# Performance work log

Hardware: AMD Instinct MI355X
Metric: run time of the kernel (lower is better)

The kernel has to match this reference:

```python
import jax, jax.numpy as jnp
import numpy as np

N_AST, M, C, D, H, OUT = 200000, 400000, 25000, 256, 4, 256


def setup_inputs() -> dict:
    key = jax.random.key(0)
    ks = jax.random.split(key, 12)
    s = 0.02
    return {
        "ast_nodes_encodings": jax.random.normal(ks[0], (N_AST, D), jnp.float32),
        "ast_node_idx_to_pdg_node_idx_mapping_key": jax.random.randint(ks[1], (M,), 0, N_AST),
        "ast_node_idx_to_pdg_node_idx_mapping_value": jax.random.randint(ks[2], (M,), 0, C),
        "pdg_node_idx_to_sub_ast_root_idx_mapping_key": jax.random.randint(ks[3], (C,), 0, C),
        "pdg_node_idx_to_sub_ast_root_idx_mapping_value": jax.random.randint(ks[4], (C,), 0, N_AST),
        "nr_cfg_nodes": C,
        "Wq": jax.random.normal(ks[5], (D, D), jnp.float32) * s,
        "bq": jnp.zeros((D,), jnp.float32),
        "Wk": jax.random.normal(ks[6], (D, D), jnp.float32) * s,
        "bk": jnp.zeros((D,), jnp.float32),
        "Wv": jax.random.normal(ks[7], (D, D), jnp.float32) * s,
        "bv": jnp.zeros((D,), jnp.float32),
        "Wo": jax.random.normal(ks[8], (D, OUT), jnp.float32) * s,
        "bo": jnp.zeros((OUT,), jnp.float32),
    }


def _scatter_attn(x, attn_keys, seg, num_segments, Wq, bq, Wk, bk, Wv, bv, Wo, bo):
    # x: [M, D] scattered inputs; attn_keys: [C, D] per-segment queries; seg: [M] segment ids.
    d_h = D // H
    q = (attn_keys @ Wq + bq).reshape(num_segments, H, d_h)  # [C,H,dh]
    k = (x @ Wk + bk).reshape(-1, H, d_h)                    # [M,H,dh]
    v = (x @ Wv + bv).reshape(-1, H, d_h)                    # [M,H,dh]
    scale = 1.0 / jnp.sqrt(jnp.asarray(d_h, x.dtype))
    scores = jnp.einsum('mhd,mhd->mh', k, q[seg]) * scale    # [M,H]
    m = jax.ops.segment_max(scores, seg, num_segments=num_segments)  # [C,H]
    e = jnp.exp(scores - m[seg])                             # [M,H]
    denom = jax.ops.segment_sum(e, seg, num_segments=num_segments)  # [C,H]
    num = jax.ops.segment_sum((e[..., None] * v).reshape(-1, H * d_h),
                              seg, num_segments=num_segments)        # [C,D]
    pooled = (num.reshape(num_segments, H, d_h) / (denom[..., None] + 1e-9)).reshape(num_segments, D)
    return pooled @ Wo + bo                                  # [C,OUT]


def reference(ast_nodes_encodings,
              ast_node_idx_to_pdg_node_idx_mapping_key,
              ast_node_idx_to_pdg_node_idx_mapping_value,
              pdg_node_idx_to_sub_ast_root_idx_mapping_key,
              pdg_node_idx_to_sub_ast_root_idx_mapping_value,
              nr_cfg_nodes, Wq, bq, Wk, bk, Wv, bv, Wo, bo):
    # Build per-CFG-node attention keys: gather sub-AST-root encodings, scatter by PDG node idx.
    root_enc = ast_nodes_encodings[pdg_node_idx_to_sub_ast_root_idx_mapping_value]  # [C,D]
    attn_keys = jnp.zeros((nr_cfg_nodes, D), ast_nodes_encodings.dtype)
    attn_keys = attn_keys.at[pdg_node_idx_to_sub_ast_root_idx_mapping_key].set(root_enc)
    # Gather AST node encodings per mapping entry and attention-pool per CFG node.
    scattered = ast_nodes_encodings[ast_node_idx_to_pdg_node_idx_mapping_key]       # [M,D]
    return _scatter_attn(scattered, attn_keys, ast_node_idx_to_pdg_node_idx_mapping_value,
                         nr_cfg_nodes, Wq, bq, Wk, bk, Wv, bv, Wo, bo)
```

## Files before the change

### kernel.cpp

```cpp
#include <hip/hip_runtime.h>
#include <hip/hip_bf16.h>
#include <math.h>

#define D 256
#define H 4
#define DH 64
#define NOUT 256

typedef short bf16x8 __attribute__((ext_vector_type(8)));
typedef float f32x4 __attribute__((ext_vector_type(4)));

__device__ __forceinline__ ushort f2bf(float f){
  uint b = __float_as_uint(f);
  b += 0x7FFF + ((b >> 16) & 1);
  return (ushort)(b >> 16);
}

__device__ __forceinline__ float redux32(float v){
  int t;
  t = __builtin_amdgcn_update_dpp(0, __float_as_int(v), 0x121, 0xF, 0xF, true); v += __int_as_float(t);
  t = __builtin_amdgcn_update_dpp(0, __float_as_int(v), 0x122, 0xF, 0xF, true); v += __int_as_float(t);
  t = __builtin_amdgcn_update_dpp(0, __float_as_int(v), 0x124, 0xF, 0xF, true); v += __int_as_float(t);
  t = __builtin_amdgcn_update_dpp(0, __float_as_int(v), 0x128, 0xF, 0xF, true); v += __int_as_float(t);
  v += __shfl_xor(v, 16, 64);
  return v;
}

__global__ void count_winner_kernel(const int* __restrict__ seg, int* __restrict__ counts,
                                    const int* __restrict__ pdgkey, int* __restrict__ winner,
                                    int M, int C){
  int i = blockIdx.x*256 + threadIdx.x;
  if (i < M){ int s = seg[i]; if (s >= 0 && s < C) atomicAdd(&counts[s], 1); }
  if (i < C){ int t = pdgkey[i]; if (t >= 0 && t < C) atomicMax(&winner[t], i); }
}

__global__ __launch_bounds__(1024) void scan1_kernel(const int* __restrict__ counts,
    int* __restrict__ loc, int* __restrict__ btot, int C){
  __shared__ int wtot[16];
  __shared__ int wexcl[16];
  int tid = threadIdx.x, lane = tid & 63, wv = tid >> 6;
  int i = blockIdx.x*1024 + tid;
  int v = (i < C) ? counts[i] : 0;
  int x = v;
  #pragma unroll
  for (int d2 = 1; d2 < 64; d2 <<= 1){
    int t = __shfl_up(x, d2, 64);
    if (lane >= d2) x += t;
  }
  if (lane == 63) wtot[wv] = x;
  __syncthreads();
  if (wv == 0 && lane < 16){
    int t = wtot[lane]; int y = t;
    #pragma unroll
    for (int d2 = 1; d2 < 16; d2 <<= 1){
      int u = __shfl_up(y, d2, 64);
      if (lane >= d2) y += u;
    }
    wexcl[lane] = y - t;
    if (lane == 15) btot[blockIdx.x] = y;
  }
  __syncthreads();
  if (i < C) loc[i] = wexcl[wv] + x - v;
}

__global__ void scan2_kernel(const int* __restrict__ btot, int* __restrict__ bexcl,
                             int nb, int* __restrict__ offsets, int C){
  int lane = threadIdx.x;
  int v = (lane < nb) ? btot[lane] : 0;
  int x = v;
  #pragma unroll
  for (int d2 = 1; d2 < 64; d2 <<= 1){
    int t = __shfl_up(x, d2, 64);
    if (lane >= d2) x += t;
  }
  if (lane < nb) bexcl[lane] = x - v;
  if (lane == 63) offsets[C] = x;
}

__global__ void scan3_kernel(const int* __restrict__ loc, const int* __restrict__ bexcl,
                             int* __restrict__ offsets, int* __restrict__ pos, int C){
  int i = blockIdx.x*256 + threadIdx.x;
  if (i < C){ int o = loc[i] + bexcl[i >> 10]; offsets[i] = o; pos[i] = o; }
}

__global__ void fill_kernel(const int* __restrict__ seg, int* __restrict__ pos,
                            int* __restrict__ members, int M, int C){
  int i = blockIdx.x*256 + threadIdx.x;
  if (i < M){ int s = seg[i]; if (s >= 0 && s < C){ int p = atomicAdd(&pos[s], 1); members[p] = i; } }
}

__global__ __launch_bounds__(256) void prep_weights(
    const float* __restrict__ Wq, const float* __restrict__ Wk,
    const float* __restrict__ Wv, const float* __restrict__ Wo,
    const float* __restrict__ bq, const float* __restrict__ bk,
    const float* __restrict__ bv,
    ushort* __restrict__ Wq16, ushort* __restrict__ Wk16, ushort* __restrict__ Wv16,
    ushort* __restrict__ WoT16,
    float* __restrict__ wqbk, float* __restrict__ bvo,
    float* __restrict__ bqk, float* __restrict__ cbh){
  __shared__ float t[64][65];
  int bid = blockIdx.x, tid = threadIdx.x;
  if (bid < 256){
    int id = bid*256 + tid;
    Wq16[id] = f2bf(Wq[id]);
    Wk16[id] = f2bf(Wk[id]);
    Wv16[id] = f2bf(Wv[id]);
  } else if (bid < 269){
    int id = (bid - 256)*256 + tid;
    if (id < 1024){
      int h = id >> 8, k = id & 255;
      float s = 0.f;
      for (int d = 0; d < DH; d++) s += Wq[(size_t)k*256 + h*64 + d] * bk[h*64 + d];
      wqbk[id] = s;
    } else if (id < 2048){
      int tt = id - 1024; int h = tt >> 8, o = tt & 255;
      float s = 0.f;
      for (int d = 0; d < DH; d++) s += bv[h*64 + d] * Wo[(size_t)(h*64 + d)*256 + o];
      bvo[tt] = s;
    } else if (id < 3072){
      int tt = id - 2048; int h = tt >> 8, e = tt & 255;
      float s = 0.f;
      for (int d = 0; d < DH; d++) s += bq[h*64 + d] * Wk[(size_t)e*256 + h*64 + d];
      bqk[tt] = s;
    } else if (id < 3076){
      int h = id - 3072;
      float s = 0.f;
      for (int d = 0; d < DH; d++) s += bq[h*64 + d] * bk[h*64 + d];
      cbh[h] = s;
    }
  } else {
    int b2 = bid - 269;
    int bx = b2 & 3, by = b2 >> 2;
    int r = tid >> 6, cc = tid & 63;
    #pragma unroll
    for (int rr = 0; rr < 64; rr += 4)
      t[rr + r][cc] = Wo[(size_t)(by*64 + rr + r)*256 + bx*64 + cc];
    __syncthreads();
    #pragma unroll
    for (int rr = 0; rr < 64; rr += 4)
      WoT16[(size_t)(bx*64 + rr + r)*256 + by*64 + cc] = f2bf(t[cc][rr + r]);
  }
}

__global__ void gather_ag(const float* __restrict__ enc, const int* __restrict__ rootval,
                          const int* __restrict__ winner, ushort* __restrict__ Ag, int C){
  int id = blockIdx.x*256 + threadIdx.x;
  if (id < C*64){
    int c = id >> 6, g = id & 63;
    int w = winner[c];
    float4 v = make_float4(0.f, 0.f, 0.f, 0.f);
    if (w >= 0) v = *(const float4*)(enc + (size_t)rootval[w]*D + g*4);
    ushort4 u; u.x = f2bf(v.x); u.y = f2bf(v.y); u.z = f2bf(v.z); u.w = f2bf(v.w);
    *(ushort4*)(Ag + (size_t)c*D + g*4) = u;
  }
}

template<bool OUT_BF16>
__global__ __launch_bounds__(256) void mfma_gemm(
    const ushort* __restrict__ A, int sA, int acol_h,
    const ushort* __restrict__ Bt, int sBt, int btrow_h, int btcol_h,
    void* __restrict__ Out, int sOut, int outrow_h, int outcol_h,
    int M, int K,
    const float* __restrict__ bias, const float* __restrict__ beta4,
    const float* __restrict__ bvo4){
  __shared__ __align__(16) ushort As[64][72];
  __shared__ __align__(16) ushort Bs[64][72];
  int tid = threadIdx.x;
  int hz = blockIdx.z;
  int m0 = blockIdx.x*64;
  int acol0  = acol_h*hz;
  int btrow0 = blockIdx.y*64 + btrow_h*hz;
  int btcol0 = btcol_h*hz;
  int outrow0 = outrow_h*hz;
  int outcol0 = blockIdx.y*64 + outcol_h*hz;
  int w = tid >> 6, lane = tid & 63, quad = lane >> 4, l16 = lane & 15;
  int r1 = tid >> 3, c8 = (tid & 7)*8;
  f32x4 acc[4] = {};
  for (int k0 = 0; k0 < K; k0 += 64){
    const ushort* ga = A + (size_t)(m0 + r1)*sA + acol0 + k0 + c8;
    uint4 v1 = make_uint4(0,0,0,0), v2 = make_uint4(0,0,0,0);
    if (m0 + r1 < M)      v1 = *(const uint4*)ga;
    if (m0 + r1 + 32 < M) v2 = *(const uint4*)(ga + (size_t)32*sA);
    *(uint4*)&As[r1][c8]      = v1;
    *(uint4*)&As[r1+32][c8]   = v2;
    const ushort* gb = Bt + (size_t)(btrow0 + r1)*sBt + btcol0 + k0 + c8;
    *(uint4*)&Bs[r1][c8]      = *(const uint4*)gb;
    *(uint4*)&Bs[r1+32][c8]   = *(const uint4*)(gb + (size_t)32*sBt);
    __syncthreads();
    #pragma unroll
    for (int ks = 0; ks < 2; ks++){
      bf16x8 b = *(const bf16x8*)&Bs[w*16 + l16][ks*32 + quad*8];
      #pragma unroll
      for (int mt = 0; mt < 4; mt++){
        bf16x8 a = *(const bf16x8*)&As[mt*16 + l16][ks*32 + quad*8];
        acc[mt] = __builtin_amdgcn_mfma_f32_16x16x32_bf16(a, b, acc[mt], 0, 0, 0);
      }
    }
    __syncthreads();
  }
  int col = outcol0 + w*16 + l16;
  int bcol = btrow0 + w*16 + l16;
  float bval = bias ? bias[bcol] : 0.f;
  #pragma unroll
  for (int mt = 0; mt < 4; mt++){
    #pragma unroll
    for (int r = 0; r < 4; r++){
      int row = m0 + mt*16 + quad*4 + r;
      if (row < M){
        float v = acc[mt][r] + bval;
        if (bvo4){
          v += beta4[row*4+0]*bvo4[0*256 + bcol] + beta4[row*4+1]*bvo4[1*256 + bcol]
             + beta4[row*4+2]*bvo4[2*256 + bcol] + beta4[row*4+3]*bvo4[3*256 + bcol];
        }
        if (OUT_BF16) ((ushort*)Out)[(size_t)(outrow0 + row)*sOut + col] = f2bf(v);
        else          ((float*)Out)[(size_t)(outrow0 + row)*sOut + col] = v;
      }
    }
  }
}

__global__ __launch_bounds__(256) void seg_attn(const float* __restrict__ enc,
    const int* __restrict__ astkey, const int* __restrict__ members,
    const int* __restrict__ offsets, const ushort* __restrict__ Ag,
    const float* __restrict__ wqbk, const float* __restrict__ cbh,
    const ushort* __restrict__ qk16, ushort* __restrict__ Shat16,
    float* __restrict__ beta, int C){
  int lane = threadIdx.x & 63, wave = threadIdx.x >> 6;
  int c = blockIdx.x*4 + wave;
  if (c >= C) return;
  int half = lane >> 5, sl = lane & 31;
  float qk[4][8];
  const ushort* qkp = qk16 + (size_t)c*1024 + sl*8;
  #pragma unroll
  for (int h = 0; h < 4; h++){
    uint4 u = *(const uint4*)(qkp + h*256);
    qk[h][0]=__uint_as_float(u.x<<16); qk[h][1]=__uint_as_float(u.x&0xffff0000u);
    qk[h][2]=__uint_as_float(u.y<<16); qk[h][3]=__uint_as_float(u.y&0xffff0000u);
    qk[h][4]=__uint_as_float(u.z<<16); qk[h][5]=__uint_as_float(u.z&0xffff0000u);
    qk[h][6]=__uint_as_float(u.w<<16); qk[h][7]=__uint_as_float(u.w&0xffff0000u);
  }
  float qbv[4];
  {
    uint4 a = *(const uint4*)(Ag + (size_t)c*256 + sl*8);
    float av[8];
    av[0]=__uint_as_float(a.x<<16); av[1]=__uint_as_float(a.x&0xffff0000u);
    av[2]=__uint_as_float(a.y<<16); av[3]=__uint_as_float(a.y&0xffff0000u);
    av[4]=__uint_as_float(a.z<<16); av[5]=__uint_as_float(a.z&0xffff0000u);
    av[6]=__uint_as_float(a.w<<16); av[7]=__uint_as_float(a.w&0xffff0000u);
    #pragma unroll
    for (int h = 0; h < 4; h++){
      const float* wp = wqbk + h*256 + sl*8;
      float p = av[0]*wp[0] + av[1]*wp[1] + av[2]*wp[2] + av[3]*wp[3]
              + av[4]*wp[4] + av[5]*wp[5] + av[6]*wp[6] + av[7]*wp[7];
      qbv[h] = redux32(p) + cbh[h];
    }
  }
  int off = offsets[c];
  int n = offsets[c+1] - off;
  float S[4][8] = {};
  float l[4] = {0.f, 0.f, 0.f, 0.f};
  for (int base = 0; base < n; base += 64){
    int cnt = min(64, n - base);
    int xrow = 0;
    if (lane < cnt) xrow = astkey[members[off + base + lane]];
    int r0 = __shfl(xrow, half, 64);
    int r1 = __shfl(xrow, 2 + half, 64);
    const float* p0 = enc + (size_t)r0*256 + sl*8;
    const float* p1 = enc + (size_t)r1*256 + sl*8;
    float4 xa0 = *(const float4*)p0, xa1 = *(const float4*)(p0 + 4);
    float4 xb0 = *(const float4*)p1, xb1 = *(const float4*)(p1 + 4);
    for (int j = 0; j < cnt; j += 4){
      float4 na0 = xa0, na1 = xa1, nb0 = xb0, nb1 = xb1;
      if (j + 4 < cnt){
        int k0 = j + 4 + half, k1 = j + 6 + half;
        int rr0 = __shfl(xrow, (k0 > 63) ? 63 : k0, 64);
        int rr1 = __shfl(xrow, (k1 > 63) ? 63 : k1, 64);
        const float* q0 = enc + (size_t)rr0*256 + sl*8;
        const float* q1 = enc + (size_t)rr1*256 + sl*8;
        na0 = *(const float4*)q0; na1 = *(const float4*)(q0 + 4);
        nb0 = *(const float4*)q1; nb1 = *(const float4*)(q1 + 4);
      }
      float xa[8] = {xa0.x, xa0.y, xa0.z, xa0.w, xa1.x, xa1.y, xa1.z, xa1.w};
      float xb[8] = {xb0.x, xb0.y, xb0.z, xb0.w, xb1.x, xb1.y, xb1.z, xb1.w};
      float pa[4], pb[4];
      #pragma unroll
      for (int h = 0; h < 4; h++){
        pa[h] = xa[0]*qk[h][0] + xa[1]*qk[h][1] + xa[2]*qk[h][2] + xa[3]*qk[h][3]
              + xa[4]*qk[h][4] + xa[5]*qk[h][5] + xa[6]*qk[h][6] + xa[7]*qk[h][7];
        pb[h] = xb[0]*qk[h][0] + xb[1]*qk[h][1] + xb[2]*qk[h][2] + xb[3]*qk[h][3]
              + xb[4]*qk[h][4] + xb[5]*qk[h][5] + xb[6]*qk[h][6] + xb[7]*qk[h][7];
      }
      #pragma unroll
      for (int h = 0; h < 4; h++){ pa[h] = redux32(pa[h]); pb[h] = redux32(pb[h]); }
      bool v0 = (j + half) < cnt;
      bool v1 = (j + 2 + half) < cnt;
      float ea[4], eb[4];
      #pragma unroll
      for (int h = 0; h < 4; h++){
        ea[h] = v0 ? __expf((pa[h] + qbv[h]) * 0.125f) : 0.f;
        eb[h] = v1 ? __expf((pb[h] + qbv[h]) * 0.125f) : 0.f;
      }
      #pragma unroll
      for (int h = 0; h < 4; h++){
        l[h] += ea[h] + eb[h];
        #pragma unroll
        for (int k = 0; k < 8; k++){
          S[h][k] += ea[h]*xa[k];
          S[h][k] += eb[h]*xb[k];
        }
      }
      xa0 = na0; xa1 = na1; xb0 = nb0; xb1 = nb1;
    }
  }
  #pragma unroll
  for (int h = 0; h < 4; h++) l[h] += __shfl_xor(l[h], 32, 64);
  #pragma unroll
  for (int h = 0; h < 4; h++){
    #pragma unroll
    for (int k = 0; k < 8; k++) S[h][k] += __shfl_xor(S[h][k], 32, 64);
  }
  float inv[4];
  #pragma unroll
  for (int h = 0; h < 4; h++) inv[h] = 1.f / (l[h] + 1e-9f);
  if (half == 0){
    ushort* sp = Shat16 + (size_t)c*1024 + sl*8;
    #pragma unroll
    for (int h = 0; h < 4; h++){
      float ih = inv[h];
      uint4 o;
      o.x = (uint)f2bf(S[h][0]*ih) | ((uint)f2bf(S[h][1]*ih) << 16);
      o.y = (uint)f2bf(S[h][2]*ih) | ((uint)f2bf(S[h][3]*ih) << 16);
      o.z = (uint)f2bf(S[h][4]*ih) | ((uint)f2bf(S[h][5]*ih) << 16);
      o.w = (uint)f2bf(S[h][6]*ih) | ((uint)f2bf(S[h][7]*ih) << 16);
      *(uint4*)(sp + h*256) = o;
    }
  }
  if (lane == 0){
    beta[c*4+0] = l[0] / (l[0] + 1e-9f);
    beta[c*4+1] = l[1] / (l[1] + 1e-9f);
    beta[c*4+2] = l[2] / (l[2] + 1e-9f);
    beta[c*4+3] = l[3] / (l[3] + 1e-9f);
  }
}

extern "C" void kernel_launch(void* const* d_in, const int* in_sizes, int n_in,
                              void* d_out, int out_size, void* d_ws, size_t ws_size,
                              hipStream_t stream) {
  const float* enc    = (const float*)d_in[0];
  const int*   astkey = (const int*)d_in[1];
  const int*   seg    = (const int*)d_in[2];
  const int*   pdgkey = (const int*)d_in[3];
  const int*   pdgval = (const int*)d_in[4];
  const float* Wq = (const float*)d_in[6];
  const float* bq = (const float*)d_in[7];
  const float* Wk = (const float*)d_in[8];
  const float* bk = (const float*)d_in[9];
  const float* Wv = (const float*)d_in[10];
  const float* bv = (const float*)d_in[11];
  const float* Wo = (const float*)d_in[12];
  const float* bo = (const float*)d_in[13];
  float* out = (float*)d_out;
  const int M = in_sizes[1];
  const int C = in_sizes[3];

  char* p = (char*)d_ws;
  auto alloc = [&](size_t bytes) -> void* {
    void* r = (void*)p;
    p += (bytes + 255) / 256 * 256;
    return r;
  };
  ushort* Ag      = (ushort*)alloc((size_t)C * D * 2);
  ushort* qk16    = (ushort*)alloc((size_t)C * H * D * 2);
  ushort* Shat16  = (ushort*)alloc((size_t)C * H * D * 2);
  float*  beta    = (float*)alloc((size_t)C * H * 4);
  ushort* Wq16    = (ushort*)alloc((size_t)D * D * 2);
  ushort* Wk16    = (ushort*)alloc((size_t)D * D * 2);
  ushort* Wv16    = (ushort*)alloc((size_t)D * D * 2);
  ushort* WoT16   = (ushort*)alloc((size_t)D * D * 2);
  ushort* Gt16    = (ushort*)alloc((size_t)H * D * D * 2);
  ushort* Zt16    = (ushort*)alloc((size_t)D * H * D * 2);
  float*  wqbk    = (float*)alloc((size_t)H * D * 4);
  float*  bvo     = (float*)alloc((size_t)H * NOUT * 4);
  float*  bqk     = (float*)alloc((size_t)H * D * 4);
  float*  cbh     = (float*)alloc((size_t)H * 4);
  int*   winner   = (int*)alloc((size_t)C * 4);
  int*   counts   = (int*)alloc((size_t)C * 4);
  int*   loc      = (int*)alloc((size_t)C * 4);
  int*   btot     = (int*)alloc((size_t)64 * 4);
  int*   bexcl    = (int*)alloc((size_t)64 * 4);
  int*   offsets  = (int*)alloc((size_t)(C + 1) * 4);
  int*   pos      = (int*)alloc((size_t)C * 4);
  int*   members  = (int*)alloc((size_t)M * 4);

  hipMemsetAsync(winner, 0xFF, (size_t)C * 4, stream);
  hipMemsetAsync(counts, 0, (size_t)C * 4, stream);

  int gC = (C + 255) / 256, gM = (M + 255) / 256;
  int gMC = ((M > C ? M : C) + 255) / 256;
  int nb1024 = (C + 1023) / 1024;
  count_winner_kernel<<<gMC, 256, 0, stream>>>(seg, counts, pdgkey, winner, M, C);
  scan1_kernel<<<nb1024, 1024, 0, stream>>>(counts, loc, btot, C);
  scan2_kernel<<<1, 64, 0, stream>>>(btot, bexcl, nb1024, offsets, C);
  scan3_kernel<<<gC, 256, 0, stream>>>(loc, bexcl, offsets, pos, C);
  fill_kernel<<<gM, 256, 0, stream>>>(seg, pos, members, M, C);

  prep_weights<<<285, 256, 0, stream>>>(Wq, Wk, Wv, Wo, bq, bk, bv,
                                        Wq16, Wk16, Wv16, WoT16, wqbk, bvo, bqk, cbh);

  mfma_gemm<true><<<dim3(4,4,4), 256, 0, stream>>>(
      Wk16, D, DH,  Wq16, D, 0, DH,  Gt16, D, D, 0,  D, DH, nullptr, nullptr, nullptr);
  mfma_gemm<true><<<dim3(4,4,4), 256, 0, stream>>>(
      WoT16, D, DH,  Wv16, D, 0, DH,  Zt16, H*D, 0, D,  D, DH, nullptr, nullptr, nullptr);

  gather_ag<<<(C*64 + 255)/256, 256, 0, stream>>>(enc, pdgval, winner, Ag, C);

  int mt = (C + 63) / 64;
  mfma_gemm<true><<<dim3(mt,4,4), 256, 0, stream>>>(
      Ag, D, 0,  Gt16, D, D, 0,  qk16, H*D, 0, D,  C, D, bqk, nullptr, nullptr);

  seg_attn<<<(C + 3)/4, 256, 0, stream>>>(enc, astkey, members, offsets, Ag,
                                          wqbk, cbh, qk16, Shat16, beta, C);

  mfma_gemm<false><<<dim3(mt,4,1), 256, 0, stream>>>(
      Shat16, H*D, 0,  Zt16, H*D, 0, 0,  out, NOUT, 0, 0,  C, H*D, bo, beta, bvo);
}
```

Before: 508.3 us.

## Assign one segment per half-wave and precompute row indices and query bias

seg_attn now gives each half-wave (32 lanes) its own CFG segment, where before a full wave handled one segment with its two halves splitting the members. This removes the final cross-half shuffle reduction and the idle half when writing. fill_kernel stores astkey[i] directly, so the attention loop does one indirect load per member instead of two. The per-segment query-bias dot products move into gather_ag, which saves qb for seg_attn to read. Segments average about 16 members, so per-segment load imbalance inside a wave and divergence between its two halves may offset some of the gain.

```diff
diff --git a/kernel.cpp b/kernel.cpp
--- a/kernel.cpp
+++ b/kernel.cpp
@@ -14,6 +14,9 @@
   uint b = __float_as_uint(f);
   b += 0x7FFF + ((b >> 16) & 1);
   return (ushort)(b >> 16);
+}
+__device__ __forceinline__ float bf2f(ushort u){
+  return __uint_as_float(((uint)u) << 16);
 }
 
 __device__ __forceinline__ float redux32(float v){
@@ -83,10 +86,13 @@
   if (i < C){ int o = loc[i] + bexcl[i >> 10]; offsets[i] = o; pos[i] = o; }
 }
 
-__global__ void fill_kernel(const int* __restrict__ seg, int* __restrict__ pos,
-                            int* __restrict__ members, int M, int C){
+__global__ void fill_kernel(const int* __restrict__ seg, const int* __restrict__ astkey,
+                            int* __restrict__ pos, int* __restrict__ rows, int M, int C){
   int i = blockIdx.x*256 + threadIdx.x;
-  if (i < M){ int s = seg[i]; if (s >= 0 && s < C){ int p = atomicAdd(&pos[s], 1); members[p] = i; } }
+  if (i < M){
+    int s = seg[i];
+    if (s >= 0 && s < C){ int p = atomicAdd(&pos[s], 1); rows[p] = astkey[i]; }
+  }
 }
 
 __global__ __launch_bounds__(256) void prep_weights(
@@ -143,16 +149,28 @@
 }
 
 __global__ void gather_ag(const float* __restrict__ enc, const int* __restrict__ rootval,
-                          const int* __restrict__ winner, ushort* __restrict__ Ag, int C){
+                          const int* __restrict__ winner,
+                          const float* __restrict__ wqbk, const float* __restrict__ cbh,
+                          ushort* __restrict__ Ag, float* __restrict__ qb, int C){
   int id = blockIdx.x*256 + threadIdx.x;
-  if (id < C*64){
-    int c = id >> 6, g = id & 63;
-    int w = winner[c];
-    float4 v = make_float4(0.f, 0.f, 0.f, 0.f);
-    if (w >= 0) v = *(const float4*)(enc + (size_t)rootval[w]*D + g*4);
-    ushort4 u; u.x = f2bf(v.x); u.y = f2bf(v.y); u.z = f2bf(v.z); u.w = f2bf(v.w);
-    *(ushort4*)(Ag + (size_t)c*D + g*4) = u;
-  }
+  int c = id >> 6, g = id & 63;
+  if (c >= C) return;
+  int w = winner[c];
+  float4 v = make_float4(0.f, 0.f, 0.f, 0.f);
+  if (w >= 0) v = *(const float4*)(enc + (size_t)rootval[w]*D + g*4);
+  ushort4 u; u.x = f2bf(v.x); u.y = f2bf(v.y); u.z = f2bf(v.z); u.w = f2bf(v.w);
+  *(ushort4*)(Ag + (size_t)c*D + g*4) = u;
+  float b0 = bf2f(u.x), b1 = bf2f(u.y), b2 = bf2f(u.z), b3 = bf2f(u.w);
+  float pv[4];
+  #pragma unroll
+  for (int h = 0; h < 4; h++){
+    float4 wv = *(const float4*)(wqbk + h*256 + g*4);
+    float p = b0*wv.x + b1*wv.y + b2*wv.z + b3*wv.w;
+    p = redux32(p);
+    p += __shfl_xor(p, 32, 64);
+    pv[h] = p;
+  }
+  if (g < 4) qb[c*4 + g] = pv[g] + cbh[g];
 }
 
 template<bool OUT_BF16>
@@ -220,15 +238,13 @@
 }
 
 __global__ __launch_bounds__(256) void seg_attn(const float* __restrict__ enc,
-    const int* __restrict__ astkey, const int* __restrict__ members,
-    const int* __restrict__ offsets, const ushort* __restrict__ Ag,
-    const float* __restrict__ wqbk, const float* __restrict__ cbh,
-    const ushort* __restrict__ qk16, ushort* __restrict__ Shat16,
-    float* __restrict__ beta, int C){
+    const int* __restrict__ rows, const int* __restrict__ offsets,
+    const ushort* __restrict__ qk16, const float* __restrict__ qb,
+    ushort* __restrict__ Shat16, float* __restrict__ beta, int C){
   int lane = threadIdx.x & 63, wave = threadIdx.x >> 6;
-  int c = blockIdx.x*4 + wave;
+  int half = lane >> 5, sl = lane & 31;
+  int c = blockIdx.x*8 + wave*2 + half;
   if (c >= C) return;
-  int half = lane >> 5, sl = lane & 31;
   float qk[4][8];
   const ushort* qkp = qk16 + (size_t)c*1024 + sl*8;
   #pragma unroll
@@ -239,42 +255,27 @@
     qk[h][4]=__uint_as_float(u.z<<16); qk[h][5]=__uint_as_float(u.z&0xffff0000u);
     qk[h][6]=__uint_as_float(u.w<<16); qk[h][7]=__uint_as_float(u.w&0xffff0000u);
   }
-  float qbv[4];
-  {
-    uint4 a = *(const uint4*)(Ag + (size_t)c*256 + sl*8);
-    float av[8];
-    av[0]=__uint_as_float(a.x<<16); av[1]=__uint_as_float(a.x&0xffff0000u);
-    av[2]=__uint_as_float(a.y<<16); av[3]=__uint_as_float(a.y&0xffff0000u);
-    av[4]=__uint_as_float(a.z<<16); av[5]=__uint_as_float(a.z&0xffff0000u);
-    av[6]=__uint_as_float(a.w<<16); av[7]=__uint_as_float(a.w&0xffff0000u);
-    #pragma unroll
-    for (int h = 0; h < 4; h++){
-      const float* wp = wqbk + h*256 + sl*8;
-      float p = av[0]*wp[0] + av[1]*wp[1] + av[2]*wp[2] + av[3]*wp[3]
-              + av[4]*wp[4] + av[5]*wp[5] + av[6]*wp[6] + av[7]*wp[7];
-      qbv[h] = redux32(p) + cbh[h];
-    }
-  }
+  float4 qbv = *(const float4*)(qb + (size_t)c*4);
+  float qbh[4] = {qbv.x, qbv.y, qbv.z, qbv.w};
   int off = offsets[c];
   int n = offsets[c+1] - off;
   float S[4][8] = {};
   float l[4] = {0.f, 0.f, 0.f, 0.f};
-  for (int base = 0; base < n; base += 64){
-    int cnt = min(64, n - base);
+  for (int base = 0; base < n; base += 32){
+    int cnt = min(32, n - base);
     int xrow = 0;
-    if (lane < cnt) xrow = astkey[members[off + base + lane]];
-    int r0 = __shfl(xrow, half, 64);
-    int r1 = __shfl(xrow, 2 + half, 64);
+    if (sl < cnt) xrow = rows[off + base + sl];
+    int r0 = __shfl(xrow, half*32 + 0, 64);
+    int r1 = __shfl(xrow, half*32 + ((cnt > 1) ? 1 : 0), 64);
     const float* p0 = enc + (size_t)r0*256 + sl*8;
     const float* p1 = enc + (size_t)r1*256 + sl*8;
     float4 xa0 = *(const float4*)p0, xa1 = *(const float4*)(p0 + 4);
     float4 xb0 = *(const float4*)p1, xb1 = *(const float4*)(p1 + 4);
-    for (int j = 0; j < cnt; j += 4){
+    for (int j = 0; j < cnt; j += 2){
       float4 na0 = xa0, na1 = xa1, nb0 = xb0, nb1 = xb1;
-      if (j + 4 < cnt){
-        int k0 = j + 4 + half, k1 = j + 6 + half;
-        int rr0 = __shfl(xrow, (k0 > 63) ? 63 : k0, 64);
-        int rr1 = __shfl(xrow, (k1 > 63) ? 63 : k1, 64);
+      if (j + 2 < cnt){
+        int rr0 = __shfl(xrow, half*32 + j + 2, 64);
+        int rr1 = __shfl(xrow, half*32 + ((j + 3 < cnt) ? (j + 3) : (j + 2)), 64);
         const float* q0 = enc + (size_t)rr0*256 + sl*8;
         const float* q1 = enc + (size_t)rr1*256 + sl*8;
         na0 = *(const float4*)q0; na1 = *(const float4*)(q0 + 4);
@@ -292,13 +293,12 @@
       }
       #pragma unroll
       for (int h = 0; h < 4; h++){ pa[h] = redux32(pa[h]); pb[h] = redux32(pb[h]); }
-      bool v0 = (j + half) < cnt;
-      bool v1 = (j + 2 + half) < cnt;
+      bool v1 = (j + 1) < cnt;
       float ea[4], eb[4];
       #pragma unroll
       for (int h = 0; h < 4; h++){
-        ea[h] = v0 ? __expf((pa[h] + qbv[h]) * 0.125f) : 0.f;
-        eb[h] = v1 ? __expf((pb[h] + qbv[h]) * 0.125f) : 0.f;
+        ea[h] = __expf((pa[h] + qbh[h]) * 0.125f);
+        eb[h] = v1 ? __expf((pb[h] + qbh[h]) * 0.125f) : 0.f;
       }
       #pragma unroll
       for (int h = 0; h < 4; h++){
@@ -312,30 +312,21 @@
       xa0 = na0; xa1 = na1; xb0 = nb0; xb1 = nb1;
     }
   }
-  #pragma unroll
-  for (int h = 0; h < 4; h++) l[h] += __shfl_xor(l[h], 32, 64);
+  float inv[4];
+  #pragma unroll
+  for (int h = 0; h < 4; h++) inv[h] = 1.f / (l[h] + 1e-9f);
+  ushort* sp = Shat16 + (size_t)c*1024 + sl*8;
   #pragma unroll
   for (int h = 0; h < 4; h++){
-    #pragma unroll
-    for (int k = 0; k < 8; k++) S[h][k] += __shfl_xor(S[h][k], 32, 64);
-  }
-  float inv[4];
-  #pragma unroll
-  for (int h = 0; h < 4; h++) inv[h] = 1.f / (l[h] + 1e-9f);
-  if (half == 0){
-    ushort* sp = Shat16 + (size_t)c*1024 + sl*8;
-    #pragma unroll
-    for (int h = 0; h < 4; h++){
-      float ih = inv[h];
-      uint4 o;
-      o.x = (uint)f2bf(S[h][0]*ih) | ((uint)f2bf(S[h][1]*ih) << 16);
-      o.y = (uint)f2bf(S[h][2]*ih) | ((uint)f2bf(S[h][3]*ih) << 16);
-      o.z = (uint)f2bf(S[h][4]*ih) | ((uint)f2bf(S[h][5]*ih) << 16);
-      o.w = (uint)f2bf(S[h][6]*ih) | ((uint)f2bf(S[h][7]*ih) << 16);
-      *(uint4*)(sp + h*256) = o;
-    }
-  }
-  if (lane == 0){
+    float ih = inv[h];
+    uint4 o;
+    o.x = (uint)f2bf(S[h][0]*ih) | ((uint)f2bf(S[h][1]*ih) << 16);
+    o.y = (uint)f2bf(S[h][2]*ih) | ((uint)f2bf(S[h][3]*ih) << 16);
+    o.z = (uint)f2bf(S[h][4]*ih) | ((uint)f2bf(S[h][5]*ih) << 16);
+    o.w = (uint)f2bf(S[h][6]*ih) | ((uint)f2bf(S[h][7]*ih) << 16);
+    *(uint4*)(sp + h*256) = o;
+  }
+  if (sl == 0){
     beta[c*4+0] = l[0] / (l[0] + 1e-9f);
     beta[c*4+1] = l[1] / (l[1] + 1e-9f);
     beta[c*4+2] = l[2] / (l[2] + 1e-9f);
@@ -373,6 +364,7 @@
   ushort* qk16    = (ushort*)alloc((size_t)C * H * D * 2);
   ushort* Shat16  = (ushort*)alloc((size_t)C * H * D * 2);
   float*  beta    = (float*)alloc((size_t)C * H * 4);
+  float*  qb      = (float*)alloc((size_t)C * H * 4);
   ushort* Wq16    = (ushort*)alloc((size_t)D * D * 2);
   ushort* Wk16    = (ushort*)alloc((size_t)D * D * 2);
   ushort* Wv16    = (ushort*)alloc((size_t)D * D * 2);
@@ -390,7 +382,7 @@
   int*   bexcl    = (int*)alloc((size_t)64 * 4);
   int*   offsets  = (int*)alloc((size_t)(C + 1) * 4);
   int*   pos      = (int*)alloc((size_t)C * 4);
-  int*   members  = (int*)alloc((size_t)M * 4);
+  int*   rows     = (int*)alloc((size_t)M * 4);
 
   hipMemsetAsync(winner, 0xFF, (size_t)C * 4, stream);
   hipMemsetAsync(counts, 0, (size_t)C * 4, stream);
@@ -402,7 +394,7 @@
   scan1_kernel<<<nb1024, 1024, 0, stream>>>(counts, loc, btot, C);
   scan2_kernel<<<1, 64, 0, stream>>>(btot, bexcl, nb1024, offsets, C);
   scan3_kernel<<<gC, 256, 0, stream>>>(loc, bexcl, offsets, pos, C);
-  fill_kernel<<<gM, 256, 0, stream>>>(seg, pos, members, M, C);
+  fill_kernel<<<gM, 256, 0, stream>>>(seg, astkey, pos, rows, M, C);
 
   prep_weights<<<285, 256, 0, stream>>>(Wq, Wk, Wv, Wo, bq, bk, bv,
                                         Wq16, Wk16, Wv16, WoT16, wqbk, bvo, bqk, cbh);
@@ -412,14 +404,15 @@
   mfma_gemm<true><<<dim3(4,4,4), 256, 0, stream>>>(
       WoT16, D, DH,  Wv16, D, 0, DH,  Zt16, H*D, 0, D,  D, DH, nullptr, nullptr, nullptr);
 
-  gather_ag<<<(C*64 + 255)/256, 256, 0, stream>>>(enc, pdgval, winner, Ag, C);
+  gather_ag<<<(C*64 + 255)/256, 256, 0, stream>>>(enc, pdgval, winner, wqbk, cbh,
+                                                  Ag, qb, C);
 
   int mt = (C + 63) / 64;
   mfma_gemm<true><<<dim3(mt,4,4), 256, 0, stream>>>(
       Ag, D, 0,  Gt16, D, D, 0,  qk16, H*D, 0, D,  C, D, bqk, nullptr, nullptr);
 
-  seg_attn<<<(C + 3)/4, 256, 0, stream>>>(enc, astkey, members, offsets, Ag,
-                                          wqbk, cbh, qk16, Shat16, beta, C);
+  seg_attn<<<(C + 7)/8, 256, 0, stream>>>(enc, rows, offsets, qk16, qb,
+                                          Shat16, beta, C);
 
   mfma_gemm<false><<<dim3(mt,4,1), 256, 0, stream>>>(
       Shat16, H*D, 0,  Zt16, H*D, 0, 0,  out, NOUT, 0, 0,  C, H*D, bo, beta, bvo);
```

After: 500.4 us. Within noise of the previous version (-1.6%).
